# Kernel tuning notes

Hardware: AMD Instinct MI355X
Metric: run time of the kernel (lower is better)

The kernel has to match this reference:

```python
import jax, jax.numpy as jnp
from jax import lax
import numpy as np

KPAD = 2  # padding for 5x5 kernel, 'same' output

def setup_inputs() -> dict:
    key = jax.random.key(0)
    x = jax.random.normal(key, (16, 8, 512, 512), dtype=jnp.float32)
    # fixed 5x5 averaging kernel, matching torch.ones(5,5)/25
    weight = jnp.ones((1, 1, 5, 5), dtype=jnp.float32) / 25.0
    return {"x": x, "weight": weight}

def reference(x, weight):
    # Per-channel (depthwise) 5x5 box blur. The torch code loops conv2d over
    # split channels; a single grouped conv with feature_group_count=C is the
    # same math in one fused op.
    C = x.shape[1]
    k = jnp.tile(weight, (C, 1, 1, 1))  # (C,1,5,5) OIHW with groups=C
    return lax.conv_general_dilated(
        x, k,
        window_strides=(1, 1),
        padding=[(KPAD, KPAD), (KPAD, KPAD)],
        dimension_numbers=("NCHW", "OIHW", "NCHW"),
        feature_group_count=C,
    )
```

## Files before the change

### kernel.cpp

```cpp
#include <hip/hip_runtime.h>


#define H 512
#define W 512
#define RSTRIP 16

__global__ __launch_bounds__(256, 4) void avefilter_kernel(
    const float* __restrict__ x, const float* __restrict__ wgt,
    float* __restrict__ out)
{
    const int lane  = threadIdx.x & 63;
    const int wave  = threadIdx.x >> 6;
    const int strip = blockIdx.x * 4 + wave;
    const int plane = strip >> 5;
    const int r0    = (strip & 31) * RSTRIP;

    const float* in   = x   + (size_t)plane * (H * W);
    float*       outp = out + (size_t)plane * (H * W);
    const float scale = wgt[0];

    const int c0 = lane * 8;

    float hr[5][8];

    auto make_h = [&](int gr, float h[8]) {
        float v[8];
        if (gr >= 0 && gr < H) {
            const float4* p = (const float4*)(in + (size_t)gr * W + c0);
            float4 a = p[0], b = p[1];
            v[0]=a.x; v[1]=a.y; v[2]=a.z; v[3]=a.w;
            v[4]=b.x; v[5]=b.y; v[6]=b.z; v[7]=b.w;
        } else {
            #pragma unroll
            for (int j = 0; j < 8; ++j) v[j] = 0.f;
        }
        float l6 = __shfl_up(v[6], 1);
        float l7 = __shfl_up(v[7], 1);
        float rA = __shfl_down(v[0], 1);
        float rB = __shfl_down(v[1], 1);
        if (lane == 0)  { l6 = 0.f; l7 = 0.f; }
        if (lane == 63) { rA = 0.f; rB = 0.f; }
        float e[12];
        e[0] = l6; e[1] = l7;
        #pragma unroll
        for (int j = 0; j < 8; ++j) e[2 + j] = v[j];
        e[10] = rA; e[11] = rB;
        #pragma unroll
        for (int j = 0; j < 8; ++j)
            h[j] = e[j] + e[j+1] + e[j+2] + e[j+3] + e[j+4];
    };

    #pragma unroll
    for (int k = 0; k < 4; ++k)
        make_h(r0 - 2 + k, hr[k]);

    #pragma unroll
    for (int r = 0; r < RSTRIP; ++r) {
        make_h(r0 + 2 + r, hr[(r + 4) % 5]);
        float o[8];
        #pragma unroll
        for (int j = 0; j < 8; ++j)
            o[j] = (hr[0][j] + hr[1][j] + hr[2][j] + hr[3][j] + hr[4][j]) * scale;
        float4* q = (float4*)(outp + (size_t)(r0 + r) * W + c0);
        q[0] = make_float4(o[0], o[1], o[2], o[3]);
        q[1] = make_float4(o[4], o[5], o[6], o[7]);
    }
}

extern "C" void kernel_launch(void* const* d_in, const int* in_sizes, int n_in,
                              void* d_out, int out_size, void* d_ws, size_t ws_size,
                              hipStream_t stream) {
    const float* x   = (const float*)d_in[0];
    const float* wgt = (const float*)d_in[1];
    float* out = (float*)d_out;

    dim3 grid(1024);
    dim3 block(256);
    avefilter_kernel<<<grid, block, 0, stream>>>(x, wgt, out);
}
```

Measured before the change: 250.7 us.

## Split rows into half-width waves with halo loads and nontemporal stores

Each wave now covers half a row (256 columns, 4 per lane) instead of a full row, which doubles the grid and raises the launch-bounds occupancy hint to 8. Lanes at the half boundary load a 2-float halo directly from global memory rather than getting it through shuffles. Output is written with nontemporal vector stores to keep streaming writes from polluting the cache. The trade-off is more redundant vertical halo reads per wave and a few extra divergent halo loads, in exchange for more waves in flight and lower register pressure.

```diff
diff --git a/kernel.cpp b/kernel.cpp
--- a/kernel.cpp
+++ b/kernel.cpp
@@ -5,49 +5,52 @@
 #define W 512
 #define RSTRIP 16
 
-__global__ __launch_bounds__(256, 4) void avefilter_kernel(
+typedef float vfloat4 __attribute__((ext_vector_type(4)));
+
+__global__ __launch_bounds__(256, 8) void avefilter_kernel(
     const float* __restrict__ x, const float* __restrict__ wgt,
     float* __restrict__ out)
 {
-    const int lane  = threadIdx.x & 63;
-    const int wave  = threadIdx.x >> 6;
-    const int strip = blockIdx.x * 4 + wave;
-    const int plane = strip >> 5;
-    const int r0    = (strip & 31) * RSTRIP;
+    const int lane = threadIdx.x & 63;
+    const int wv   = threadIdx.x >> 6;
+    const int g    = blockIdx.x * 4 + wv;
+    const int plane = g >> 6;
+    const int s     = g & 63;
+    const int half  = s & 1;
+    const int strip = s >> 1;
+    const int r0    = strip * RSTRIP;
+    const int col0  = half * 256;
 
     const float* in   = x   + (size_t)plane * (H * W);
     float*       outp = out + (size_t)plane * (H * W);
     const float scale = wgt[0];
 
-    const int c0 = lane * 8;
+    const int c = col0 + lane * 4;
 
-    float hr[5][8];
+    float hr[5][4];
 
-    auto make_h = [&](int gr, float h[8]) {
-        float v[8];
+    auto make_h = [&](int gr, float h[4]) {
+        float4 v  = make_float4(0.f, 0.f, 0.f, 0.f);
+        float2 lh = make_float2(0.f, 0.f);
+        float2 rh = make_float2(0.f, 0.f);
         if (gr >= 0 && gr < H) {
-            const float4* p = (const float4*)(in + (size_t)gr * W + c0);
-            float4 a = p[0], b = p[1];
-            v[0]=a.x; v[1]=a.y; v[2]=a.z; v[3]=a.w;
-            v[4]=b.x; v[5]=b.y; v[6]=b.z; v[7]=b.w;
-        } else {
-            #pragma unroll
-            for (int j = 0; j < 8; ++j) v[j] = 0.f;
+            const float* rowp = in + (size_t)gr * W;
+            v = *(const float4*)(rowp + c);
+            if (lane == 0 && col0 > 0)
+                lh = *(const float2*)(rowp + col0 - 2);
+            if (lane == 63 && col0 + 256 < W)
+                rh = *(const float2*)(rowp + col0 + 256);
         }
-        float l6 = __shfl_up(v[6], 1);
-        float l7 = __shfl_up(v[7], 1);
-        float rA = __shfl_down(v[0], 1);
-        float rB = __shfl_down(v[1], 1);
-        if (lane == 0)  { l6 = 0.f; l7 = 0.f; }
-        if (lane == 63) { rA = 0.f; rB = 0.f; }
-        float e[12];
-        e[0] = l6; e[1] = l7;
-        #pragma unroll
-        for (int j = 0; j < 8; ++j) e[2 + j] = v[j];
-        e[10] = rA; e[11] = rB;
-        #pragma unroll
-        for (int j = 0; j < 8; ++j)
-            h[j] = e[j] + e[j+1] + e[j+2] + e[j+3] + e[j+4];
+        float l2  = __shfl_up(v.z, 1);
+        float l3  = __shfl_up(v.w, 1);
+        float rr0 = __shfl_down(v.x, 1);
+        float rr1 = __shfl_down(v.y, 1);
+        if (lane == 0)  { l2 = lh.x;  l3 = lh.y; }
+        if (lane == 63) { rr0 = rh.x; rr1 = rh.y; }
+        h[0] = l2  + l3  + v.x + v.y + v.z;
+        h[1] = l3  + v.x + v.y + v.z + v.w;
+        h[2] = v.x + v.y + v.z + v.w + rr0;
+        h[3] = v.y + v.z + v.w + rr0 + rr1;
     };
 
     #pragma unroll
@@ -57,13 +60,11 @@
     #pragma unroll
     for (int r = 0; r < RSTRIP; ++r) {
         make_h(r0 + 2 + r, hr[(r + 4) % 5]);
-        float o[8];
+        vfloat4 o;
         #pragma unroll
-        for (int j = 0; j < 8; ++j)
+        for (int j = 0; j < 4; ++j)
             o[j] = (hr[0][j] + hr[1][j] + hr[2][j] + hr[3][j] + hr[4][j]) * scale;
-        float4* q = (float4*)(outp + (size_t)(r0 + r) * W + c0);
-        q[0] = make_float4(o[0], o[1], o[2], o[3]);
-        q[1] = make_float4(o[4], o[5], o[6], o[7]);
+        __builtin_nontemporal_store(o, (vfloat4*)(outp + (size_t)(r0 + r) * W + c));
     }
 }
 
@@ -74,7 +75,7 @@
     const float* wgt = (const float*)d_in[1];
     float* out = (float*)d_out;
 
-    dim3 grid(1024);
+    dim3 grid(2048);
     dim3 block(256);
     avefilter_kernel<<<grid, block, 0, stream>>>(x, wgt, out);
 }
```

Result: faster. 244.3 us (-2.5%).
